# Kernel optimization log

Measured on AMD Instinct MI355X. Metric: run time of the kernel, lower is better.

The kernel has to match this reference:

```python
import jax, jax.numpy as jnp
import numpy as np

D_IN = 512
D = 1024      # new_embed_dim
H = 16        # num_heads
HD = D // H   # head_dim


def setup_inputs() -> dict:
    key = jax.random.key(0)
    ks = jax.random.split(key, 16)
    g = lambda k, shape, fan: jax.random.normal(k, shape, jnp.float32) / np.sqrt(fan)
    return {
        "x1": jax.random.normal(ks[0], (16, 1, D_IN), jnp.float32),
        "x2": jax.random.normal(ks[1], (16, 4096, D_IN), jnp.float32),
        "x3": jax.random.normal(ks[2], (16, 4096, D_IN), jnp.float32),
        # embedding1 (for x1) and embedding2 (used for BOTH x2 and x3, per source)
        "We1": g(ks[3], (D_IN, D), D_IN), "be1": jnp.zeros((D,), jnp.float32),
        "We2": g(ks[4], (D_IN, D), D_IN), "be2": jnp.zeros((D,), jnp.float32),
        "Wq": g(ks[5], (D, D), D), "bq": jnp.zeros((D,), jnp.float32),
        "Wk": g(ks[6], (D, D), D), "bk": jnp.zeros((D,), jnp.float32),
        "Wv": g(ks[7], (D, D), D), "bv": jnp.zeros((D,), jnp.float32),
        "Wo": g(ks[8], (D, D), D), "bo": jnp.zeros((D,), jnp.float32),
    }


def reference(x1, x2, x3, We1, be1, We2, be2, Wq, bq, Wk, bk, Wv, bv, Wo, bo):
    B = x1.shape[0]
    # embeddings (x3 intentionally uses embedding2's weights, matching source)
    x1e = x1 @ We1 + be1                      # [B,1,D]
    x2e = x2 @ We2 + be2                      # [B,S,D]
    x3e = x3 @ We2 + be2                      # [B,S,D]
    q = (x1e @ Wq + bq).reshape(B, -1, H, HD).transpose(0, 2, 1, 3)  # [B,H,1,HD]
    k = (x2e @ Wk + bk).reshape(B, -1, H, HD).transpose(0, 2, 1, 3)  # [B,H,S,HD]
    v = (x3e @ Wv + bv).reshape(B, -1, H, HD).transpose(0, 2, 1, 3)  # [B,H,S,HD]
    scale = jnp.asarray(np.sqrt(HD), q.dtype)
    attn = jax.nn.softmax(jnp.einsum("bhqd,bhkd->bhqk", q, k) / scale, axis=-1)
    # dropout is identity at inference (keras training=False default)
    av = jnp.einsum("bhqk,bhkd->bhqd", attn, v)          # [B,H,1,HD]
    av = av.transpose(0, 2, 1, 3).reshape(B, -1, D)      # [B,1,D]
    out = av @ Wo + bo                                   # [B,1,D]
    return jnp.squeeze(out, axis=1)                      # [B,D]
```

## Files before the change

kernel.cpp:

```cpp
#include <hip/hip_runtime.h>


#define DIN 512
#define DD  1024
#define NH  16
#define HD  64
#define BB  16
#define SS  4096

__device__ __forceinline__ int wave_id() {
    return __builtin_amdgcn_readfirstlane((int)(threadIdx.x >> 6));
}

__global__ __launch_bounds__(256) void k_transpose(const float* __restrict__ in,
                                                   float* __restrict__ out,
                                                   int R, int C) {
    __shared__ float tl[32][33];
    const int tx = threadIdx.x & 31, ty = threadIdx.x >> 5;
    const int c0 = blockIdx.x * 32, r0 = blockIdx.y * 32;
#pragma unroll
    for (int k = 0; k < 4; ++k) {
        int r = r0 + ty + k * 8;
        tl[ty + k * 8][tx] = in[(size_t)r * C + c0 + tx];
    }
    __syncthreads();
#pragma unroll
    for (int k = 0; k < 4; ++k) {
        int c = c0 + ty + k * 8;
        out[(size_t)c * R + r0 + tx] = tl[tx][ty + k * 8];
    }
}

__global__ __launch_bounds__(256) void k_init(const float* __restrict__ be1,
                                              const float* __restrict__ bq,
                                              const float* __restrict__ bv,
                                              const float* __restrict__ bo,
                                              float* __restrict__ x1e,
                                              float* __restrict__ qb,
                                              float* __restrict__ av,
                                              float* __restrict__ out) {
    const int b = blockIdx.x;
#pragma unroll
    for (int k = 0; k < 4; ++k) {
        const int c = k * 256 + threadIdx.x;
        x1e[(size_t)b * DD + c] = be1[c];
        qb[(size_t)b * DD + c]  = bq[c];
        av[(size_t)b * DD + c]  = bv[c];
        out[(size_t)b * DD + c] = bo[c];
    }
}

template <int K, int N, int KS, bool HASB>
__global__ __launch_bounds__(256) void k_bmv2(const float* __restrict__ in,
                                              const float* __restrict__ W,
                                              const float* __restrict__ bias,
                                              float* __restrict__ out) {
    const int l = threadIdx.x & 63;
    const int c = blockIdx.x * 64 + l;
    const int wv = wave_id();
    constexpr int KCH = K / KS;
    constexpr int SUB = KCH / 4;
    const float* inb = in + (size_t)blockIdx.y * 16 * K;
    float acc[16];
#pragma unroll
    for (int r = 0; r < 16; ++r) acc[r] = 0.f;
    const int i0 = blockIdx.z * KCH + wv * SUB;
#pragma unroll 4
    for (int i = i0; i < i0 + SUB; ++i) {
        const float wval = W[(size_t)i * N + c];
#pragma unroll
        for (int r = 0; r < 16; ++r) acc[r] += inb[(size_t)r * K + i] * wval;
    }
    __shared__ float red[4][16][64];
#pragma unroll
    for (int r = 0; r < 16; ++r) red[wv][r][l] = acc[r];
    __syncthreads();
#pragma unroll
    for (int k = 0; k < 4; ++k) {
        const int r = wv + k * 4;
        float v = red[0][r][l] + red[1][r][l] + red[2][r][l] + red[3][r][l];
        float* dst = out + ((size_t)blockIdx.y * 16 + r) * N + c;
        if (KS == 1) {
            if (HASB) v += bias[c];
            *dst = v;
        } else {
            atomicAdd(dst, v);
        }
    }
}

__global__ __launch_bounds__(256) void k_u2(const float* __restrict__ q,
                                            const float* __restrict__ WkT,
                                            float* __restrict__ u) {
    const int h = blockIdx.y;
    const int l = threadIdx.x & 63;
    const int c = blockIdx.x * 64 + l;
    const int wv = wave_id();
    float acc[16];
#pragma unroll
    for (int bb = 0; bb < 16; ++bb) acc[bb] = 0.f;
#pragma unroll 4
    for (int dk = 0; dk < 16; ++dk) {
        const int d = wv * 16 + dk;
        const float wval = WkT[(size_t)(h * HD + d) * DD + c];
#pragma unroll
        for (int bb = 0; bb < 16; ++bb)
            acc[bb] += q[(size_t)bb * DD + h * HD + d] * wval;
    }
    __shared__ float red[4][16][64];
#pragma unroll
    for (int bb = 0; bb < 16; ++bb) red[wv][bb][l] = acc[bb];
    __syncthreads();
#pragma unroll
    for (int k = 0; k < 4; ++k) {
        const int bb = wv + k * 4;
        float v = red[0][bb][l] + red[1][bb][l] + red[2][bb][l] + red[3][bb][l];
        u[((size_t)bb * NH + h) * DD + c] = v;
    }
}

__global__ __launch_bounds__(256) void k_scores(const float* __restrict__ x2,
                                                const float* __restrict__ w,
                                                float* __restrict__ sc) {
    __shared__ float4 tile[64 * 32];
    const int b = blockIdx.y;
    const int s0 = blockIdx.x * 64;
    const int l = threadIdx.x & 63;
    const int h0 = wave_id() * 4;
    const float4* x2f = (const float4*)x2 + ((size_t)b * SS + s0) * (DIN / 4);
    float a0 = 0.f, a1 = 0.f, a2 = 0.f, a3 = 0.f;
#pragma unroll
    for (int kt = 0; kt < 4; ++kt) {
#pragma unroll
        for (int k = 0; k < 8; ++k) {
            const int j = threadIdx.x + k * 256;
            const int row = j >> 5, c4 = j & 31;
            tile[row * 32 + (c4 ^ (row & 7))] = x2f[row * (DIN / 4) + kt * 32 + c4];
        }
        __syncthreads();
        const float4* wp = (const float4*)(w + ((size_t)b * NH + h0) * DIN + kt * 128);
#pragma unroll 8
        for (int c4 = 0; c4 < 32; ++c4) {
            const float4 x = tile[l * 32 + (c4 ^ (l & 7))];
            const float4 q0 = wp[c4];
            const float4 q1 = wp[128 + c4];
            const float4 q2 = wp[256 + c4];
            const float4 q3 = wp[384 + c4];
            a0 += x.x * q0.x + x.y * q0.y + x.z * q0.z + x.w * q0.w;
            a1 += x.x * q1.x + x.y * q1.y + x.z * q1.z + x.w * q1.w;
            a2 += x.x * q2.x + x.y * q2.y + x.z * q2.z + x.w * q2.w;
            a3 += x.x * q3.x + x.y * q3.y + x.z * q3.z + x.w * q3.w;
        }
        __syncthreads();
    }
    const size_t base = ((size_t)b * NH + h0) * SS + s0 + l;
    sc[base + 0 * SS] = a0;
    sc[base + 1 * SS] = a1;
    sc[base + 2 * SS] = a2;
    sc[base + 3 * SS] = a3;
}

__global__ __launch_bounds__(256) void k_softmax(float* __restrict__ sc) {
    float4* row = (float4*)(sc + (size_t)blockIdx.x * SS);
    float4 v[4];
    float m = -1e30f;
#pragma unroll
    for (int j = 0; j < 4; ++j) {
        v[j] = row[threadIdx.x + j * 256];
        m = fmaxf(m, fmaxf(fmaxf(v[j].x, v[j].y), fmaxf(v[j].z, v[j].w)));
    }
    __shared__ float red[256];
    red[threadIdx.x] = m;
    __syncthreads();
    for (int s = 128; s > 0; s >>= 1) {
        if (threadIdx.x < (unsigned)s)
            red[threadIdx.x] = fmaxf(red[threadIdx.x], red[threadIdx.x + s]);
        __syncthreads();
    }
    m = red[0];
    __syncthreads();
    float sum = 0.f;
#pragma unroll
    for (int j = 0; j < 4; ++j) {
        v[j].x = expf((v[j].x - m) * 0.125f);
        v[j].y = expf((v[j].y - m) * 0.125f);
        v[j].z = expf((v[j].z - m) * 0.125f);
        v[j].w = expf((v[j].w - m) * 0.125f);
        sum += v[j].x + v[j].y + v[j].z + v[j].w;
    }
    red[threadIdx.x] = sum;
    __syncthreads();
    for (int s = 128; s > 0; s >>= 1) {
        if (threadIdx.x < (unsigned)s) red[threadIdx.x] += red[threadIdx.x + s];
        __syncthreads();
    }
    const float inv = 1.f / red[0];
#pragma unroll
    for (int j = 0; j < 4; ++j) {
        v[j].x *= inv; v[j].y *= inv; v[j].z *= inv; v[j].w *= inv;
        row[threadIdx.x + j * 256] = v[j];
    }
}

__global__ __launch_bounds__(256) void k_gpart(const float* __restrict__ x3,
                                               const float* __restrict__ a,
                                               float* __restrict__ gp,
                                               int schunk, int nch) {
    const int b = blockIdx.y, ch = blockIdx.x;
    const int wv = wave_id();
    const int l = threadIdx.x & 63;
    const int sub = schunk >> 2;
    const int sbeg = ch * schunk + wv * sub;
    const float* ar = a + (size_t)b * NH * SS;
    float acc[16][8];
#pragma unroll
    for (int h = 0; h < 16; ++h)
#pragma unroll
        for (int j = 0; j < 8; ++j) acc[h][j] = 0.f;

    for (int s = sbeg; s < sbeg + sub; ++s) {
        const float4* xr = (const float4*)(x3 + ((size_t)b * SS + s) * DIN);
        const float4 xa = xr[l];
        const float4 xb = xr[l + 64];
        const float xv[8] = {xa.x, xa.y, xa.z, xa.w, xb.x, xb.y, xb.z, xb.w};
#pragma unroll
        for (int h = 0; h < 16; ++h) {
            const float wh = ar[h * SS + s];
#pragma unroll
            for (int j = 0; j < 8; ++j) acc[h][j] += wh * xv[j];
        }
    }

    __shared__ float red[4][2048];
    for (int hg = 0; hg < 4; ++hg) {
        __syncthreads();
#pragma unroll
        for (int hh = 0; hh < 4; ++hh) {
            float* dst = &red[wv][hh * 512];
            const int hs = hg * 4 + hh;
            *(float4*)(dst + l * 4) =
                make_float4(acc[hs][0], acc[hs][1], acc[hs][2], acc[hs][3]);
            *(float4*)(dst + 256 + l * 4) =
                make_float4(acc[hs][4], acc[hs][5], acc[hs][6], acc[hs][7]);
        }
        __syncthreads();
        const int idx = threadIdx.x * 8;
        float o[8];
#pragma unroll
        for (int j = 0; j < 8; ++j)
            o[j] = red[0][idx + j] + red[1][idx + j] + red[2][idx + j] + red[3][idx + j];
        const int hh = idx >> 9;
        const int i = idx & 511;
        float* dst = gp + (((size_t)(b * nch + ch) * NH) + hg * 4 + hh) * DIN + i;
        *(float4*)dst = make_float4(o[0], o[1], o[2], o[3]);
        *(float4*)(dst + 4) = make_float4(o[4], o[5], o[6], o[7]);
    }
}

__global__ __launch_bounds__(256) void k_greduce(const float* __restrict__ gp, int nch,
                                                 float* __restrict__ g) {
    const int pair = blockIdx.x;
    const int b = pair >> 4, h = pair & 15;
#pragma unroll
    for (int kk = 0; kk < 2; ++kk) {
        const int i = kk * 256 + threadIdx.x;
        float acc = 0.f;
        for (int ch = 0; ch < nch; ++ch)
            acc += gp[((size_t)(b * nch + ch) * NH + h) * DIN + i];
        g[(size_t)pair * DIN + i] = acc;
    }
}

__global__ __launch_bounds__(256) void k_av_at(const float* __restrict__ G2,
                                               const float* __restrict__ Wv,
                                               float* __restrict__ av) {
    const int h = blockIdx.x;
    const int l = threadIdx.x & 63;
    const int wv = wave_id();
    const int c0 = blockIdx.y * 128 + wv * 32;
    float acc[16];
#pragma unroll
    for (int bb = 0; bb < 16; ++bb) acc[bb] = 0.f;
#pragma unroll 4
    for (int c = c0; c < c0 + 32; ++c) {
        const float wval = Wv[(size_t)c * DD + h * HD + l];
#pragma unroll
        for (int bb = 0; bb < 16; ++bb)
            acc[bb] += G2[((size_t)bb * NH + h) * DD + c] * wval;
    }
    __shared__ float red[4][16][64];
#pragma unroll
    for (int bb = 0; bb < 16; ++bb) red[wv][bb][l] = acc[bb];
    __syncthreads();
#pragma unroll
    for (int k = 0; k < 4; ++k) {
        const int bb = wv + k * 4;
        float v = red[0][bb][l] + red[1][bb][l] + red[2][bb][l] + red[3][bb][l];
        atomicAdd(&av[(size_t)bb * DD + h * HD + l], v);
    }
}

extern "C" void kernel_launch(void* const* d_in, const int* in_sizes, int n_in,
                              void* d_out, int out_size, void* d_ws, size_t ws_size,
                              hipStream_t stream) {
    const float* x1  = (const float*)d_in[0];
    const float* x2  = (const float*)d_in[1];
    const float* x3  = (const float*)d_in[2];
    const float* We1 = (const float*)d_in[3];
    const float* be1 = (const float*)d_in[4];
    const float* We2 = (const float*)d_in[5];
    const float* be2 = (const float*)d_in[6];
    const float* Wq  = (const float*)d_in[7];
    const float* bq  = (const float*)d_in[8];
    const float* Wk  = (const float*)d_in[9];
    const float* bk  = (const float*)d_in[10];
    const float* Wv  = (const float*)d_in[11];
    const float* bv  = (const float*)d_in[12];
    const float* Wo  = (const float*)d_in[13];
    const float* bo  = (const float*)d_in[14];
    (void)bk;
    float* out = (float*)d_out;

    char* ws = (char*)d_ws;
    size_t off = 0;
    auto alloc = [&](size_t bytes) -> void* {
        void* p = ws + off;
        off = (off + bytes + 255) & ~(size_t)255;
        return p;
    };
    float* We2t = (float*)alloc((size_t)DD * DIN * 4);
    float* WkT  = (float*)alloc((size_t)DD * DD * 4);
    float* x1e  = (float*)alloc((size_t)BB * DD * 4);
    float* qb   = (float*)alloc((size_t)BB * DD * 4);
    float* u    = (float*)alloc((size_t)BB * NH * DD * 4);
    float* wv_  = (float*)alloc((size_t)BB * NH * DIN * 4);
    float* sc   = (float*)alloc((size_t)BB * NH * SS * 4);
    float* g    = (float*)alloc((size_t)BB * NH * DIN * 4);
    float* G2   = (float*)alloc((size_t)BB * NH * DD * 4);
    float* av   = (float*)alloc((size_t)BB * DD * 4);

    const size_t per_chunk = (size_t)BB * NH * DIN * 4;
    int nch = 32;
    while (nch > 8 && off + (size_t)nch * per_chunk > ws_size) nch >>= 1;
    float* gp = (float*)alloc((size_t)nch * per_chunk);
    const int schunk = SS / nch;

    k_transpose<<<dim3(DD / 32, DIN / 32), 256, 0, stream>>>(We2, We2t, DIN, DD);
    k_transpose<<<dim3(DD / 32, DD / 32), 256, 0, stream>>>(Wk, WkT, DD, DD);
    k_init<<<BB, 256, 0, stream>>>(be1, bq, bv, bo, x1e, qb, av, out);
    k_bmv2<DIN, DD, 8, false><<<dim3(DD / 64, 1, 8), 256, 0, stream>>>(x1, We1, nullptr, x1e);
    k_bmv2<DD, DD, 8, false><<<dim3(DD / 64, 1, 8), 256, 0, stream>>>(x1e, Wq, nullptr, qb);
    k_u2<<<dim3(DD / 64, NH), 256, 0, stream>>>(qb, WkT, u);
    k_bmv2<DD, DIN, 1, false><<<dim3(DIN / 64, BB * NH / 16, 1), 256, 0, stream>>>(u, We2t, nullptr, wv_);
    k_scores<<<dim3(SS / 64, BB), 256, 0, stream>>>(x2, wv_, sc);
    k_softmax<<<BB * NH, 256, 0, stream>>>(sc);
    k_gpart<<<dim3(nch, BB), 256, 0, stream>>>(x3, sc, gp, schunk, nch);
    k_greduce<<<BB * NH, 256, 0, stream>>>(gp, nch, g);
    k_bmv2<DIN, DD, 1, true><<<dim3(DD / 64, BB * NH / 16, 1), 256, 0, stream>>>(g, We2, be2, G2);
    k_av_at<<<dim3(NH, 8), 256, 0, stream>>>(G2, Wv, av);
    k_bmv2<DD, DD, 8, false><<<dim3(DD / 64, 1, 8), 256, 0, stream>>>(av, Wo, nullptr, out);
}
```

Baseline: 462.6 us.

## Merge prep kernels, pad scores LDS tile, unroll gpart sequence loop

Combines the two weight transposes and the bias-init kernel into a single launch, selecting the work by block index, to cut launch overhead. In k_scores the XOR-swizzled LDS tile is replaced by a padded 33-stride layout, the kt loop is no longer unrolled, and the barriers are moved. k_gpart's sequence loop is unrolled by 2 to raise memory-level parallelism. The padding changes the LDS bank-conflict pattern for float4 reads and may help or hurt, and the unroll adds register pressure on top of a 128-float accumulator array.

```diff
diff --git a/kernel.cpp b/kernel.cpp
--- a/kernel.cpp
+++ b/kernel.cpp
@@ -12,41 +12,49 @@
     return __builtin_amdgcn_readfirstlane((int)(threadIdx.x >> 6));
 }
 
-__global__ __launch_bounds__(256) void k_transpose(const float* __restrict__ in,
-                                                   float* __restrict__ out,
-                                                   int R, int C) {
+__device__ __forceinline__ void tile_transpose(const float* __restrict__ in,
+                                               float* __restrict__ out,
+                                               int R, int C, int rblk, int cblk) {
     __shared__ float tl[32][33];
     const int tx = threadIdx.x & 31, ty = threadIdx.x >> 5;
-    const int c0 = blockIdx.x * 32, r0 = blockIdx.y * 32;
-#pragma unroll
-    for (int k = 0; k < 4; ++k) {
-        int r = r0 + ty + k * 8;
-        tl[ty + k * 8][tx] = in[(size_t)r * C + c0 + tx];
-    }
-    __syncthreads();
-#pragma unroll
-    for (int k = 0; k < 4; ++k) {
-        int c = c0 + ty + k * 8;
-        out[(size_t)c * R + r0 + tx] = tl[tx][ty + k * 8];
-    }
-}
-
-__global__ __launch_bounds__(256) void k_init(const float* __restrict__ be1,
+    const int c0 = cblk * 32, r0 = rblk * 32;
+#pragma unroll
+    for (int k = 0; k < 4; ++k)
+        tl[ty + k * 8][tx] = in[(size_t)(r0 + ty + k * 8) * C + c0 + tx];
+    __syncthreads();
+#pragma unroll
+    for (int k = 0; k < 4; ++k)
+        out[(size_t)(c0 + ty + k * 8) * R + r0 + tx] = tl[tx][ty + k * 8];
+}
+
+__global__ __launch_bounds__(256) void k_prep(const float* __restrict__ We2,
+                                              const float* __restrict__ Wk,
+                                              const float* __restrict__ be1,
                                               const float* __restrict__ bq,
                                               const float* __restrict__ bv,
                                               const float* __restrict__ bo,
+                                              float* __restrict__ We2t,
+                                              float* __restrict__ WkT,
                                               float* __restrict__ x1e,
                                               float* __restrict__ qb,
                                               float* __restrict__ av,
                                               float* __restrict__ out) {
-    const int b = blockIdx.x;
-#pragma unroll
-    for (int k = 0; k < 4; ++k) {
-        const int c = k * 256 + threadIdx.x;
-        x1e[(size_t)b * DD + c] = be1[c];
-        qb[(size_t)b * DD + c]  = bq[c];
-        av[(size_t)b * DD + c]  = bv[c];
-        out[(size_t)b * DD + c] = bo[c];
+    const int bx = blockIdx.x;
+    if (bx < 512) {
+        tile_transpose(We2, We2t, DIN, DD, bx >> 5, bx & 31);
+    } else if (bx < 1536) {
+        const int lb = bx - 512;
+        tile_transpose(Wk, WkT, DD, DD, lb >> 5, lb & 31);
+    } else {
+        const int b = bx - 1536;
+#pragma unroll
+        for (int k = 0; k < 4; ++k) {
+            const int c = k * 256 + threadIdx.x;
+            x1e[(size_t)b * DD + c] = be1[c];
+            qb[(size_t)b * DD + c]  = bq[c];
+            av[(size_t)b * DD + c]  = bv[c];
+            out[(size_t)b * DD + c] = bo[c];
+        }
     }
 }
 
@@ -122,36 +130,35 @@
 __global__ __launch_bounds__(256) void k_scores(const float* __restrict__ x2,
                                                 const float* __restrict__ w,
                                                 float* __restrict__ sc) {
-    __shared__ float4 tile[64 * 32];
+    __shared__ float4 tile[64 * 33];
     const int b = blockIdx.y;
     const int s0 = blockIdx.x * 64;
     const int l = threadIdx.x & 63;
     const int h0 = wave_id() * 4;
     const float4* x2f = (const float4*)x2 + ((size_t)b * SS + s0) * (DIN / 4);
+    const float4* wp = (const float4*)(w + ((size_t)b * NH + h0) * DIN);
     float a0 = 0.f, a1 = 0.f, a2 = 0.f, a3 = 0.f;
-#pragma unroll
     for (int kt = 0; kt < 4; ++kt) {
+        __syncthreads();
 #pragma unroll
         for (int k = 0; k < 8; ++k) {
-            const int j = threadIdx.x + k * 256;
-            const int row = j >> 5, c4 = j & 31;
-            tile[row * 32 + (c4 ^ (row & 7))] = x2f[row * (DIN / 4) + kt * 32 + c4];
-        }
-        __syncthreads();
-        const float4* wp = (const float4*)(w + ((size_t)b * NH + h0) * DIN + kt * 128);
+            const int idx = threadIdx.x + k * 256;
+            const int row = idx >> 5, c4 = idx & 31;
+            tile[row * 33 + c4] = x2f[row * (DIN / 4) + kt * 32 + c4];
+        }
+        __syncthreads();
 #pragma unroll 8
         for (int c4 = 0; c4 < 32; ++c4) {
-            const float4 x = tile[l * 32 + (c4 ^ (l & 7))];
-            const float4 q0 = wp[c4];
-            const float4 q1 = wp[128 + c4];
-            const float4 q2 = wp[256 + c4];
-            const float4 q3 = wp[384 + c4];
+            const float4 x = tile[l * 33 + c4];
+            const float4 q0 = wp[kt * 32 + c4];
+            const float4 q1 = wp[128 + kt * 32 + c4];
+            const float4 q2 = wp[256 + kt * 32 + c4];
+            const float4 q3 = wp[384 + kt * 32 + c4];
             a0 += x.x * q0.x + x.y * q0.y + x.z * q0.z + x.w * q0.w;
             a1 += x.x * q1.x + x.y * q1.y + x.z * q1.z + x.w * q1.w;
             a2 += x.x * q2.x + x.y * q2.y + x.z * q2.z + x.w * q2.w;
             a3 += x.x * q3.x + x.y * q3.y + x.z * q3.z + x.w * q3.w;
         }
-        __syncthreads();
     }
     const size_t base = ((size_t)b * NH + h0) * SS + s0 + l;
     sc[base + 0 * SS] = a0;
@@ -218,6 +225,7 @@
 #pragma unroll
         for (int j = 0; j < 8; ++j) acc[h][j] = 0.f;
 
+#pragma unroll 2
     for (int s = sbeg; s < sbeg + sub; ++s) {
         const float4* xr = (const float4*)(x3 + ((size_t)b * SS + s) * DIN);
         const float4 xa = xr[l];
@@ -345,9 +353,8 @@
     float* gp = (float*)alloc((size_t)nch * per_chunk);
     const int schunk = SS / nch;
 
-    k_transpose<<<dim3(DD / 32, DIN / 32), 256, 0, stream>>>(We2, We2t, DIN, DD);
-    k_transpose<<<dim3(DD / 32, DD / 32), 256, 0, stream>>>(Wk, WkT, DD, DD);
-    k_init<<<BB, 256, 0, stream>>>(be1, bq, bv, bo, x1e, qb, av, out);
+    k_prep<<<1552, 256, 0, stream>>>(We2, Wk, be1, bq, bv, bo,
+                                     We2t, WkT, x1e, qb, av, out);
     k_bmv2<DIN, DD, 8, false><<<dim3(DD / 64, 1, 8), 256, 0, stream>>>(x1, We1, nullptr, x1e);
     k_bmv2<DD, DD, 8, false><<<dim3(DD / 64, 1, 8), 256, 0, stream>>>(x1e, Wq, nullptr, qb);
     k_u2<<<dim3(DD / 64, NH), 256, 0, stream>>>(qb, WkT, u);
```

New measurement: 465.8 us. About the same (+0.7%).
